# Optimization experiments

Hardware: AMD Instinct MI355X
Metric: run time of the kernel (lower is better)

The kernel has to match this reference:

```python
import jax, jax.numpy as jnp
import numpy as np

N = 8000          # nodes
E = 256000        # edges (avg_degree 32)
C = 64            # channels (num_channel == num_channel_hidden)
R = 8             # num_radial_basis
H = 64            # radial MLP hidden width
NPATH = 11        # (l1,l2)->lout Cartesian tensor-product paths
AVG_NUM_NEIGHBORS = 32.0


def setup_inputs() -> dict:
    key = jax.random.key(0)
    ks = jax.random.split(key, 19)
    rn = lambda k, shp, s=1.0: jax.random.normal(k, shp, dtype=jnp.float32) * s
    inp = {
        # node features per irrep order r: [N, C, (3,)*r]
        't0': rn(ks[0], (N, C)),
        't1': rn(ks[1], (N, C, 3)),
        't2': rn(ks[2], (N, C, 3, 3)),
        # edge Cartesian attrs per order l1
        'a0': rn(ks[3], (E,)),
        'a1': rn(ks[4], (E, 3)),
        'a2': rn(ks[5], (E, 3, 3)),
        'edge_feats': rn(ks[6], (E, R)),
        'cutoff': jax.random.uniform(ks[7], (E, 1), dtype=jnp.float32),
        # linear_up (SelfInteraction) channel-mix weights per l
        'W0': rn(ks[8], (C, C), 1.0 / np.sqrt(C)),
        'W1': rn(ks[9], (C, C), 1.0 / np.sqrt(C)),
        'W2': rn(ks[10], (C, C), 1.0 / np.sqrt(C)),
        # radial MLP: R -> H -> H -> H -> NPATH*C
        'Wr0': rn(ks[11], (R, H), 1.0 / np.sqrt(R)),
        'Wr1': rn(ks[12], (H, H), 1.0 / np.sqrt(H)),
        'Wr2': rn(ks[13], (H, H), 1.0 / np.sqrt(H)),
        'Wr3': rn(ks[14], (H, NPATH * C), 1.0 / np.sqrt(H)),
        # ICTD symmetrization matrices D_{l,l,1}: [3^l, 3^l] buffers
        'D0': rn(ks[15], (1, 1)),
        'D1': rn(ks[16], (3, 3)),
        'D2': rn(ks[17], (9, 9)),
        'edge_index': jax.random.randint(ks[18], (2, E), 0, N),
    }
    return inp


def reference(t0, t1, t2, a0, a1, a2, edge_feats, cutoff,
              W0, W1, W2, Wr0, Wr1, Wr2, Wr3, D0, D1, D2, edge_index):
    src, dst = edge_index[0], edge_index[1]

    # linear_up: per-irrep channel mixing
    u0 = jnp.einsum('nc,cd->nd', t0, W0)
    u1 = jnp.einsum('nci,cd->ndi', t1, W1)
    u2 = jnp.einsum('ncij,cd->ndij', t2, W2)

    # gather sender features per edge
    s0, s1, s2 = u0[src], u1[src], u2[src]

    # radial_net: per-edge path weights, gated by cutoff
    h = jax.nn.silu(edge_feats @ Wr0)
    h = jax.nn.silu(h @ Wr1)
    h = jax.nn.silu(h @ Wr2)
    w = ((h @ Wr3) * cutoff).reshape(E, NPATH, C)
    w = jnp.moveaxis(w, 1, 0)  # [NPATH, E, C]

    # Cartesian tensor-product paths (l1=edge attr order, l2=node feat order)
    # lout = 0 paths
    e0 = (w[0] * (a0[:, None] * s0)
          + w[1] * jnp.einsum('ei,eci->ec', a1, s1)
          + w[2] * jnp.einsum('eij,ecij->ec', a2, s2))
    # lout = 1 paths
    e1 = (w[3][..., None] * (a1[:, None, :] * s0[..., None])
          + w[4][..., None] * (a0[:, None, None] * s1)
          + w[5][..., None] * jnp.einsum('eij,ecj->eci', a2, s1)
          + w[6][..., None] * jnp.einsum('ej,ecij->eci', a1, s2))
    # lout = 2 paths
    e2 = (w[7][..., None, None] * jnp.einsum('ei,ecj->ecij', a1, s1)
          + w[8][..., None, None] * (a2[:, None] * s0[..., None, None])
          + w[9][..., None, None] * (a0[:, None, None, None] * s2)
          + w[10][..., None, None] * jnp.einsum('eik,eckj->ecij', a2, s2))

    # scatter-add to target nodes, normalize by avg_num_neighbors
    m0 = jax.ops.segment_sum(e0, dst, num_segments=N) / AVG_NUM_NEIGHBORS
    m1 = jax.ops.segment_sum(e1, dst, num_segments=N) / AVG_NUM_NEIGHBORS
    m2 = jax.ops.segment_sum(e2, dst, num_segments=N) / AVG_NUM_NEIGHBORS

    # apply D_{l,l,1} symmetrization on flattened last dims
    m0 = (m0.reshape(N, C, 1) @ D0).reshape(N, C)
    m1 = jnp.einsum('nci,ij->ncj', m1, D1)
    m2 = (m2.reshape(N, C, 9) @ D2).reshape(N, C, 3, 3)
    return (m0, m1, m2)
```

## Files before the change

kernel.cpp:

```cpp
#include <hip/hip_runtime.h>


#define NN 8000
#define NE 256000
#define OFF1 512000
#define OFF2 2048000

typedef __attribute__((ext_vector_type(8))) short short8;
typedef __attribute__((ext_vector_type(4))) float f32x4;
typedef __attribute__((ext_vector_type(2))) unsigned int uint2v;

__device__ __forceinline__ float silu_f(float x) {
    return x / (1.f + __expf(-x));
}
__device__ __forceinline__ unsigned short f2bf(float x) {
    unsigned int u = __float_as_uint(x);
    u += 0x7fff + ((u >> 16) & 1);
    return (unsigned short)(u >> 16);
}
__device__ __forceinline__ float bf2f(short x) {
    return __uint_as_float(((unsigned int)(unsigned short)x) << 16);
}

__global__ void k_prep(const int* __restrict__ ei, int* __restrict__ counts,
                       const float* __restrict__ Wr3, unsigned short* __restrict__ wr3t,
                       const float* __restrict__ Wr1, const float* __restrict__ Wr2,
                       unsigned short* __restrict__ wr1t, unsigned short* __restrict__ wr2t) {
    int b = blockIdx.x;
    if (b < 1000) {
        int e = b * 256 + threadIdx.x;
        atomicAdd(&counts[ei[NE + e]], 1);
    } else if (b < 1176) {
        int idx = (b - 1000) * 256 + threadIdx.x;
        if (idx < 704 * 64) {
            int n = idx >> 6, h = idx & 63;
            wr3t[idx] = f2bf(Wr3[h * 704 + n]);
        }
    } else {
        int idx = (b - 1176) * 256 + threadIdx.x;
        if (idx < 4096) {
            int j = idx >> 6, q = idx & 63;
            wr1t[idx] = f2bf(Wr1[q * 64 + j]);
            wr2t[idx] = f2bf(Wr2[q * 64 + j]);
        }
    }
}

__global__ __launch_bounds__(1024) void k_scan(const int* __restrict__ counts,
                                               int* __restrict__ row_ptr,
                                               int* __restrict__ cursor) {
    __shared__ int ssum[1024];
    int tid = threadIdx.x;
    int base = tid * 8;
    int v[8];
    int s = 0;
#pragma unroll
    for (int i = 0; i < 8; ++i) {
        int g = base + i;
        int x = (g < NN) ? counts[g] : 0;
        v[i] = s;
        s += x;
    }
    ssum[tid] = s;
    __syncthreads();
    for (int off = 1; off < 1024; off <<= 1) {
        int t = (tid >= off) ? ssum[tid - off] : 0;
        __syncthreads();
        ssum[tid] += t;
        __syncthreads();
    }
    int excl = ssum[tid] - s;
#pragma unroll
    for (int i = 0; i < 8; ++i) {
        int g = base + i;
        if (g < NN) {
            int val = excl + v[i];
            row_ptr[g] = val;
            cursor[g]  = val;
        }
    }
    if (tid == 0) row_ptr[NN] = NE;
}

__global__ void k_scatter(const int* __restrict__ ei, int* __restrict__ cursor,
                          int* __restrict__ sorted_eid) {
    int e = blockIdx.x * 256 + threadIdx.x;
    if (e < NE) {
        int pos = atomicAdd(&cursor[ei[NE + e]], 1);
        sorted_eid[pos] = e;
    }
}

__global__ __launch_bounds__(256) void k_linear_up(
    const float* __restrict__ t0, const float* __restrict__ t1,
    const float* __restrict__ t2, const float* __restrict__ W0,
    const float* __restrict__ W1, const float* __restrict__ W2,
    unsigned short* __restrict__ u16) {
    int lane = threadIdx.x & 63;
    int n = blockIdx.x * 4 + (threadIdx.x >> 6);
    if (n >= NN) return;
    float acc[13];
#pragma unroll
    for (int i = 0; i < 13; ++i) acc[i] = 0.f;
    const float* t0r = t0 + n * 64;
    const float* t1r = t1 + n * 192;
    const float* t2r = t2 + n * 576;
    for (int cin = 0; cin < 64; ++cin) {
        float w0 = W0[cin * 64 + lane];
        float w1 = W1[cin * 64 + lane];
        float w2 = W2[cin * 64 + lane];
        acc[0] = fmaf(t0r[cin], w0, acc[0]);
#pragma unroll
        for (int i = 0; i < 3; ++i)
            acc[1 + i] = fmaf(t1r[cin * 3 + i], w1, acc[1 + i]);
#pragma unroll
        for (int q = 0; q < 9; ++q)
            acc[4 + q] = fmaf(t2r[cin * 9 + q], w2, acc[4 + q]);
    }
    short8 lo, hi;
#pragma unroll
    for (int m = 0; m < 8; ++m) lo[m] = (short)f2bf(acc[m]);
#pragma unroll
    for (int m = 8; m < 13; ++m) hi[m - 8] = (short)f2bf(acc[m]);
    hi[5] = 0; hi[6] = 0; hi[7] = 0;
    short8* dst = (short8*)(u16 + (size_t)n * 1024 + lane * 16);
    dst[0] = lo;
    dst[1] = hi;
}

__global__ __launch_bounds__(256) void k_mlp(
    const int* __restrict__ sorted, const int* __restrict__ ei,
    const float* __restrict__ ef, const float* __restrict__ cut,
    const float* __restrict__ a0, const float* __restrict__ a1,
    const float* __restrict__ a2, const float* __restrict__ Wr0,
    const unsigned short* __restrict__ wr1t, const unsigned short* __restrict__ wr2t,
    unsigned short* __restrict__ h3s, float* __restrict__ a_s,
    int* __restrict__ src_s) {
    __shared__ __attribute__((aligned(16))) unsigned short h1[64 * 64];
    __shared__ __attribute__((aligned(16))) unsigned short h2[64 * 64];
    __shared__ int eid_l[64];
    __shared__ float cut_l[64];
    int tid = threadIdx.x;
    int c = tid & 63, sg = tid >> 6, jb = sg * 16;
    int l15 = c & 15, lg = c >> 4;
    int i0 = blockIdx.x * 64;

    if (tid < 64) {
        int eid = sorted[i0 + tid];
        eid_l[tid] = eid;
        src_s[i0 + tid] = ei[eid];
        cut_l[tid] = cut[eid];
    }
    __syncthreads();
    for (int idx = tid; idx < 64 * 13; idx += 256) {
        int k = idx / 13, m = idx - 13 * k;
        int eid = eid_l[k];
        float v = (m == 0) ? a0[eid]
                : (m < 4)  ? a1[(size_t)eid * 3 + (m - 1)]
                           : a2[(size_t)eid * 9 + (m - 4)];
        a_s[(size_t)(i0 + k) * 16 + m] = v;
    }
    for (int idx = tid; idx < 64 * 3; idx += 256) {
        int k = idx / 3, m = 13 + (idx - 3 * k);
        a_s[(size_t)(i0 + k) * 16 + m] = 0.f;
    }

    short8 W1f[4][2], W2f[4][2];
#pragma unroll
    for (int mt = 0; mt < 4; ++mt)
#pragma unroll
        for (int kf = 0; kf < 2; ++kf) {
            W1f[mt][kf] = *(const short8*)(wr1t + (mt * 16 + l15) * 64 + kf * 32 + lg * 8);
            W2f[mt][kf] = *(const short8*)(wr2t + (mt * 16 + l15) * 64 + kf * 32 + lg * 8);
        }

    {
        int eid = eid_l[c];
        const float* er = ef + (size_t)eid * 8;
        float ev[8];
#pragma unroll
        for (int r = 0; r < 8; ++r) ev[r] = er[r];
        float acc[16];
#pragma unroll
        for (int j = 0; j < 16; ++j) acc[j] = 0.f;
#pragma unroll
        for (int r = 0; r < 8; ++r)
#pragma unroll
            for (int j = 0; j < 16; ++j)
                acc[j] = fmaf(ev[r], Wr0[r * 64 + jb + j], acc[j]);
        int sw = (c & 7) << 4;
#pragma unroll
        for (int g = 0; g < 4; ++g) {
            uint2v pk;
            pk[0] = (unsigned int)f2bf(silu_f(acc[4 * g]))
                  | ((unsigned int)f2bf(silu_f(acc[4 * g + 1])) << 16);
            pk[1] = (unsigned int)f2bf(silu_f(acc[4 * g + 2]))
                  | ((unsigned int)f2bf(silu_f(acc[4 * g + 3])) << 16);
            int byte = (c * 128 + (jb + 4 * g) * 2) ^ sw;
            *(uint2v*)((char*)h1 + byte) = pk;
        }
    }
    __syncthreads();

    int e = sg * 16 + l15;
    int rb = e * 128;
    int sw = (e & 7) << 4;
    float cv = cut_l[e];
    {
        short8 B0 = *(const short8*)((char*)h1 + ((rb + lg * 16) ^ sw));
        short8 B1 = *(const short8*)((char*)h1 + ((rb + 64 + lg * 16) ^ sw));
        f32x4 d0 = {0.f, 0.f, 0.f, 0.f}, d1 = {0.f, 0.f, 0.f, 0.f};
        f32x4 d2 = {0.f, 0.f, 0.f, 0.f}, d3 = {0.f, 0.f, 0.f, 0.f};
        d0 = __builtin_amdgcn_mfma_f32_16x16x32_bf16(W1f[0][0], B0, d0, 0, 0, 0);
        d0 = __builtin_amdgcn_mfma_f32_16x16x32_bf16(W1f[0][1], B1, d0, 0, 0, 0);
        d1 = __builtin_amdgcn_mfma_f32_16x16x32_bf16(W1f[1][0], B0, d1, 0, 0, 0);
        d1 = __builtin_amdgcn_mfma_f32_16x16x32_bf16(W1f[1][1], B1, d1, 0, 0, 0);
        d2 = __builtin_amdgcn_mfma_f32_16x16x32_bf16(W1f[2][0], B0, d2, 0, 0, 0);
        d2 = __builtin_amdgcn_mfma_f32_16x16x32_bf16(W1f[2][1], B1, d2, 0, 0, 0);
        d3 = __builtin_amdgcn_mfma_f32_16x16x32_bf16(W1f[3][0], B0, d3, 0, 0, 0);
        d3 = __builtin_amdgcn_mfma_f32_16x16x32_bf16(W1f[3][1], B1, d3, 0, 0, 0);
        f32x4 dd[4] = {d0, d1, d2, d3};
#pragma unroll
        for (int mt = 0; mt < 4; ++mt) {
            uint2v pk;
            pk[0] = (unsigned int)f2bf(silu_f(dd[mt][0]))
                  | ((unsigned int)f2bf(silu_f(dd[mt][1])) << 16);
            pk[1] = (unsigned int)f2bf(silu_f(dd[mt][2]))
                  | ((unsigned int)f2bf(silu_f(dd[mt][3])) << 16);
            int byte = (rb + (mt * 16 + lg * 4) * 2) ^ sw;
            *(uint2v*)((char*)h2 + byte) = pk;
        }
    }
    {
        short8 B0 = *(const short8*)((char*)h2 + ((rb + lg * 16) ^ sw));
        short8 B1 = *(const short8*)((char*)h2 + ((rb + 64 + lg * 16) ^ sw));
        f32x4 d0 = {0.f, 0.f, 0.f, 0.f}, d1 = {0.f, 0.f, 0.f, 0.f};
        f32x4 d2 = {0.f, 0.f, 0.f, 0.f}, d3 = {0.f, 0.f, 0.f, 0.f};
        d0 = __builtin_amdgcn_mfma_f32_16x16x32_bf16(W2f[0][0], B0, d0, 0, 0, 0);
        d0 = __builtin_amdgcn_mfma_f32_16x16x32_bf16(W2f[0][1], B1, d0, 0, 0, 0);
        d1 = __builtin_amdgcn_mfma_f32_16x16x32_bf16(W2f[1][0], B0, d1, 0, 0, 0);
        d1 = __builtin_amdgcn_mfma_f32_16x16x32_bf16(W2f[1][1], B1, d1, 0, 0, 0);
        d2 = __builtin_amdgcn_mfma_f32_16x16x32_bf16(W2f[2][0], B0, d2, 0, 0, 0);
        d2 = __builtin_amdgcn_mfma_f32_16x16x32_bf16(W2f[2][1], B1, d2, 0, 0, 0);
        d3 = __builtin_amdgcn_mfma_f32_16x16x32_bf16(W2f[3][0], B0, d3, 0, 0, 0);
        d3 = __builtin_amdgcn_mfma_f32_16x16x32_bf16(W2f[3][1], B1, d3, 0, 0, 0);
        f32x4 dd[4] = {d0, d1, d2, d3};
#pragma unroll
        for (int mt = 0; mt < 4; ++mt) {
            uint2v pk;
            pk[0] = (unsigned int)f2bf(silu_f(dd[mt][0]) * cv)
                  | ((unsigned int)f2bf(silu_f(dd[mt][1]) * cv) << 16);
            pk[1] = (unsigned int)f2bf(silu_f(dd[mt][2]) * cv)
                  | ((unsigned int)f2bf(silu_f(dd[mt][3]) * cv) << 16);
            int byte = rb + (mt * 16 + lg * 4) * 2;
            *(uint2v*)((char*)h1 + byte) = pk;
        }
    }
    __syncthreads();
    {
        short8* dst = (short8*)(h3s + (size_t)i0 * 64);
        const short8* srcp = (const short8*)h1;
#pragma unroll
        for (int i = 0; i < 2; ++i) dst[tid + 256 * i] = srcp[tid + 256 * i];
    }
}

__global__ __launch_bounds__(256) void k_main(
    const unsigned short* __restrict__ u16, const int* __restrict__ row_ptr,
    const unsigned short* __restrict__ h3s, const float* __restrict__ a_s,
    const int* __restrict__ src_s, const unsigned short* __restrict__ wr3t,
    const float* __restrict__ D0, const float* __restrict__ D1,
    const float* __restrict__ D2, float* __restrict__ out) {
    __shared__ float red[4 * 13 * 64];
    __shared__ float m_l[13 * 64];

    int tid = threadIdx.x;
    int c = tid & 63;
    int sg = tid >> 6;
    int l15 = c & 15;
    int lg = c >> 4;
    int n = blockIdx.x;
    int beg = row_ptr[n], end = row_ptr[n + 1];
    int last = end - 1;

    int p0, p1, p2;
    if (sg == 0)      { p0 = 0; p1 = 3;  p2 = 8;  }
    else if (sg == 1) { p0 = 1; p1 = 4;  p2 = 7;  }
    else if (sg == 2) { p0 = 2; p1 = 9;  p2 = 6;  }
    else              { p0 = 5; p1 = 10; p2 = 10; }

    for (int cg = 0; cg < 4; ++cg) {
        int c_lane = cg * 16 + l15;
        const unsigned short* b0 = wr3t + (size_t)(p0 * 64 + c_lane) * 64 + lg * 8;
        const unsigned short* b1 = wr3t + (size_t)(p1 * 64 + c_lane) * 64 + lg * 8;
        const unsigned short* b2 = wr3t + (size_t)(p2 * 64 + c_lane) * 64 + lg * 8;

        float accm[13];
#pragma unroll
        for (int i = 0; i < 13; ++i) accm[i] = 0.f;

        for (int tb = beg; tb < end; tb += 16) {
            int rowc = min(tb + l15, last);
            const short8* ap = (const short8*)(h3s + (size_t)rowc * 64);
            short8 Af0 = ap[lg];
            short8 Af1 = ap[4 + lg];
            short8 Bf00 = *(const short8*)(b0);
            short8 Bf01 = *(const short8*)(b0 + 32);
            short8 Bf10 = *(const short8*)(b1);
            short8 Bf11 = *(const short8*)(b1 + 32);
            short8 Bf20 = *(const short8*)(b2);
            short8 Bf21 = *(const short8*)(b2 + 32);
            int gbase = tb + lg * 4;
            int gpc[4];
            short8 ulo[4];
#pragma unroll
            for (int r = 0; r < 4; ++r) {
                gpc[r] = min(gbase + r, last);
                ulo[r] = *(const short8*)(
                    u16 + (size_t)src_s[gpc[r]] * 1024 + c_lane * 16);
            }
            f32x4 w0v = {0.f, 0.f, 0.f, 0.f};
            f32x4 w1v = {0.f, 0.f, 0.f, 0.f};
            f32x4 w2v = {0.f, 0.f, 0.f, 0.f};
            w0v = __builtin_amdgcn_mfma_f32_16x16x32_bf16(Af0, Bf00, w0v, 0, 0, 0);
            w0v = __builtin_amdgcn_mfma_f32_16x16x32_bf16(Af1, Bf01, w0v, 0, 0, 0);
            w1v = __builtin_amdgcn_mfma_f32_16x16x32_bf16(Af0, Bf10, w1v, 0, 0, 0);
            w1v = __builtin_amdgcn_mfma_f32_16x16x32_bf16(Af1, Bf11, w1v, 0, 0, 0);
            w2v = __builtin_amdgcn_mfma_f32_16x16x32_bf16(Af0, Bf20, w2v, 0, 0, 0);
            w2v = __builtin_amdgcn_mfma_f32_16x16x32_bf16(Af1, Bf21, w2v, 0, 0, 0);
#pragma unroll
            for (int r = 0; r < 4; ++r) {
                int gp = gbase + r;
                float cv = (gp < end) ? 1.f : 0.f;
                float w0 = w0v[r] * cv;
                float w1 = w1v[r] * cv;
                float w2 = w2v[r] * cv;
                const unsigned short* uptr =
                    u16 + (size_t)src_s[gpc[r]] * 1024 + c_lane * 16;
                short8 ul = ulo[r];
                const float* av = a_s + (size_t)gpc[r] * 16;
                f32x4 q0 = *(const f32x4*)(av);
                f32x4 q1 = *(const f32x4*)(av + 4);
                f32x4 q2 = *(const f32x4*)(av + 8);
                float q3 = av[12];
                float ar[13] = {q0[0], q0[1], q0[2], q0[3],
                                q1[0], q1[1], q1[2], q1[3],
                                q2[0], q2[1], q2[2], q2[3], q3};
                if (sg == 0) {
                    float s0v = bf2f(ul[0]);
                    accm[0] = fmaf(w0 * ar[0], s0v, accm[0]);
#pragma unroll
                    for (int i3 = 0; i3 < 3; ++i3)
                        accm[1 + i3] = fmaf(w1 * ar[1 + i3], s0v, accm[1 + i3]);
#pragma unroll
                    for (int q = 0; q < 9; ++q)
                        accm[4 + q] = fmaf(w2 * ar[4 + q], s0v, accm[4 + q]);
                } else if (sg == 1) {
                    float s1v[3] = { bf2f(ul[1]), bf2f(ul[2]), bf2f(ul[3]) };
                    float d = ar[1] * s1v[0] + ar[2] * s1v[1] + ar[3] * s1v[2];
                    accm[0] = fmaf(w0, d, accm[0]);
                    float a0v = ar[0];
#pragma unroll
                    for (int i3 = 0; i3 < 3; ++i3)
                        accm[1 + i3] = fmaf(w1 * a0v, s1v[i3], accm[1 + i3]);
#pragma unroll
                    for (int i3 = 0; i3 < 3; ++i3)
#pragma unroll
                        for (int j3 = 0; j3 < 3; ++j3)
                            accm[4 + 3 * i3 + j3] =
                                fmaf(w2 * ar[1 + i3], s1v[j3], accm[4 + 3 * i3 + j3]);
                } else if (sg == 2) {
                    short8 uh = *(const short8*)(uptr + 8);
                    float s2v[9];
#pragma unroll
                    for (int q = 0; q < 9; ++q)
                        s2v[q] = (q < 4) ? bf2f(ul[4 + q]) : bf2f(uh[q - 4]);
                    float d = 0.f;
#pragma unroll
                    for (int q = 0; q < 9; ++q) d = fmaf(ar[4 + q], s2v[q], d);
                    accm[0] = fmaf(w0, d, accm[0]);
                    float a0v = ar[0];
#pragma unroll
                    for (int q = 0; q < 9; ++q)
                        accm[4 + q] = fmaf(w1 * a0v, s2v[q], accm[4 + q]);
#pragma unroll
                    for (int i3 = 0; i3 < 3; ++i3) {
                        float t = ar[1] * s2v[3 * i3] + ar[2] * s2v[3 * i3 + 1] +
                                  ar[3] * s2v[3 * i3 + 2];
                        accm[1 + i3] = fmaf(w2, t, accm[1 + i3]);
                    }
                } else {
                    short8 uh = *(const short8*)(uptr + 8);
                    float s1v[3] = { bf2f(ul[1]), bf2f(ul[2]), bf2f(ul[3]) };
                    float s2v[9];
#pragma unroll
                    for (int q = 0; q < 9; ++q)
                        s2v[q] = (q < 4) ? bf2f(ul[4 + q]) : bf2f(uh[q - 4]);
#pragma unroll
                    for (int i3 = 0; i3 < 3; ++i3) {
                        float t = ar[4 + 3 * i3] * s1v[0] + ar[4 + 3 * i3 + 1] * s1v[1] +
                                  ar[4 + 3 * i3 + 2] * s1v[2];
                        accm[1 + i3] = fmaf(w0, t, accm[1 + i3]);
                    }
#pragma unroll
                    for (int i3 = 0; i3 < 3; ++i3)
#pragma unroll
                        for (int j3 = 0; j3 < 3; ++j3) {
                            float t = ar[4 + 3 * i3] * s2v[j3] +
                                      ar[4 + 3 * i3 + 1] * s2v[3 + j3] +
                                      ar[4 + 3 * i3 + 2] * s2v[6 + j3];
                            accm[4 + 3 * i3 + j3] = fmaf(w1, t, accm[4 + 3 * i3 + j3]);
                        }
                }
            }
        }
#pragma unroll
        for (int m = 0; m < 13; ++m) {
            float v = accm[m];
            v += __shfl_xor(v, 16, 64);
            v += __shfl_xor(v, 32, 64);
            if (lg == 0) red[(sg * 13 + m) * 64 + c_lane] = v;
        }
    }

    __syncthreads();
    for (int m = sg; m < 13; m += 4) {
        float s = red[m * 64 + c] + red[(13 + m) * 64 + c] +
                  red[(26 + m) * 64 + c] + red[(39 + m) * 64 + c];
        m_l[m * 64 + c] = s * (1.f / 32.f);
    }
    __syncthreads();
    if (sg == 0) {
        out[n * 64 + c] = m_l[c] * D0[0];
    } else if (sg == 1) {
        float v0 = m_l[64 + c], v1 = m_l[128 + c], v2 = m_l[192 + c];
#pragma unroll
        for (int j = 0; j < 3; ++j) {
            float s = v0 * D1[j] + v1 * D1[3 + j] + v2 * D1[6 + j];
            out[OFF1 + (n * 64 + c) * 3 + j] = s;
        }
    } else {
        float v[9];
#pragma unroll
        for (int p = 0; p < 9; ++p) v[p] = m_l[(4 + p) * 64 + c];
        int q0 = (sg == 2) ? 0 : 5;
        int q1 = (sg == 2) ? 5 : 9;
        for (int q = q0; q < q1; ++q) {
            float s = 0.f;
#pragma unroll
            for (int p = 0; p < 9; ++p) s = fmaf(v[p], D2[p * 9 + q], s);
            out[OFF2 + (n * 64 + c) * 9 + q] = s;
        }
    }
}

extern "C" void kernel_launch(void* const* d_in, const int* in_sizes, int n_in,
                              void* d_out, int out_size, void* d_ws, size_t ws_size,
                              hipStream_t stream) {
    const float* t0 = (const float*)d_in[0];
    const float* t1 = (const float*)d_in[1];
    const float* t2 = (const float*)d_in[2];
    const float* a0 = (const float*)d_in[3];
    const float* a1 = (const float*)d_in[4];
    const float* a2 = (const float*)d_in[5];
    const float* ef = (const float*)d_in[6];
    const float* cut = (const float*)d_in[7];
    const float* W0 = (const float*)d_in[8];
    const float* W1 = (const float*)d_in[9];
    const float* W2 = (const float*)d_in[10];
    const float* Wr0 = (const float*)d_in[11];
    const float* Wr1 = (const float*)d_in[12];
    const float* Wr2 = (const float*)d_in[13];
    const float* Wr3 = (const float*)d_in[14];
    const float* D0 = (const float*)d_in[15];
    const float* D1 = (const float*)d_in[16];
    const float* D2 = (const float*)d_in[17];
    const int* ei = (const int*)d_in[18];
    float* out = (float*)d_out;

    unsigned short* u16 = (unsigned short*)d_ws;
    unsigned short* h3s = u16 + (size_t)NN * 1024;
    float* a_s = (float*)(h3s + (size_t)NE * 64);
    int* src_s = (int*)(a_s + (size_t)NE * 16);
    int* counts = src_s + NE;
    int* row_ptr = counts + NN;
    int* cursor = row_ptr + NN + 1;
    int* sorted = cursor + NN;
    unsigned short* wr3t = (unsigned short*)(sorted + NE);
    unsigned short* wr1t = wr3t + 45056;
    unsigned short* wr2t = wr1t + 4096;

    hipMemsetAsync(counts, 0, NN * sizeof(int), stream);
    k_prep<<<1192, 256, 0, stream>>>(ei, counts, Wr3, wr3t, Wr1, Wr2, wr1t, wr2t);
    k_scan<<<1, 1024, 0, stream>>>(counts, row_ptr, cursor);
    k_scatter<<<(NE + 255) / 256, 256, 0, stream>>>(ei, cursor, sorted);
    k_linear_up<<<NN / 4, 256, 0, stream>>>(t0, t1, t2, W0, W1, W2, u16);
    k_mlp<<<NE / 64, 256, 0, stream>>>(sorted, ei, ef, cut, a0, a1, a2,
                                       Wr0, wr1t, wr2t, h3s, a_s, src_s);
    k_main<<<NN, 256, 0, stream>>>(u16, row_ptr, h3s, a_s, src_s, wr3t,
                                   D0, D1, D2, out);
}
```

Baseline: 622.0 us.

## Split channels across waves instead of paths to remove cross-wave reduction

Each wave now owns a 16-channel group and computes all 11 paths for it, where before each wave handled a subset of paths and looped over all four channel groups. This removes the 4x channel-group loop, the redundant per-wave gathers of edge attributes and sender features, and the shared-memory cross-wave reduction with its extra barrier. In exchange each wave issues 22 MFMAs per edge tile and holds more weight fragments live, which raises register pressure. Wave-divergent branching on the wave index is gone.

Measured after the change: 595.8 us. -4.2%, faster.

```diff
diff --git a/kernel.cpp b/kernel.cpp
--- a/kernel.cpp
+++ b/kernel.cpp
@@ -271,7 +271,6 @@
     const int* __restrict__ src_s, const unsigned short* __restrict__ wr3t,
     const float* __restrict__ D0, const float* __restrict__ D1,
     const float* __restrict__ D2, float* __restrict__ out) {
-    __shared__ float red[4 * 13 * 64];
     __shared__ float m_l[13 * 64];
 
     int tid = threadIdx.x;
@@ -282,154 +281,149 @@
     int n = blockIdx.x;
     int beg = row_ptr[n], end = row_ptr[n + 1];
     int last = end - 1;
-
-    int p0, p1, p2;
-    if (sg == 0)      { p0 = 0; p1 = 3;  p2 = 8;  }
-    else if (sg == 1) { p0 = 1; p1 = 4;  p2 = 7;  }
-    else if (sg == 2) { p0 = 2; p1 = 9;  p2 = 6;  }
-    else              { p0 = 5; p1 = 10; p2 = 10; }
-
-    for (int cg = 0; cg < 4; ++cg) {
-        int c_lane = cg * 16 + l15;
-        const unsigned short* b0 = wr3t + (size_t)(p0 * 64 + c_lane) * 64 + lg * 8;
-        const unsigned short* b1 = wr3t + (size_t)(p1 * 64 + c_lane) * 64 + lg * 8;
-        const unsigned short* b2 = wr3t + (size_t)(p2 * 64 + c_lane) * 64 + lg * 8;
-
-        float accm[13];
-#pragma unroll
-        for (int i = 0; i < 13; ++i) accm[i] = 0.f;
-
-        for (int tb = beg; tb < end; tb += 16) {
-            int rowc = min(tb + l15, last);
-            const short8* ap = (const short8*)(h3s + (size_t)rowc * 64);
-            short8 Af0 = ap[lg];
-            short8 Af1 = ap[4 + lg];
-            short8 Bf00 = *(const short8*)(b0);
-            short8 Bf01 = *(const short8*)(b0 + 32);
-            short8 Bf10 = *(const short8*)(b1);
-            short8 Bf11 = *(const short8*)(b1 + 32);
-            short8 Bf20 = *(const short8*)(b2);
-            short8 Bf21 = *(const short8*)(b2 + 32);
-            int gbase = tb + lg * 4;
-            int gpc[4];
-            short8 ulo[4];
-#pragma unroll
-            for (int r = 0; r < 4; ++r) {
-                gpc[r] = min(gbase + r, last);
-                ulo[r] = *(const short8*)(
-                    u16 + (size_t)src_s[gpc[r]] * 1024 + c_lane * 16);
+    int c_lane = sg * 16 + l15;
+
+    float accm[13];
+#pragma unroll
+    for (int i = 0; i < 13; ++i) accm[i] = 0.f;
+
+    for (int tb = beg; tb < end; tb += 16) {
+        int rowc = min(tb + l15, last);
+        const short8* ap = (const short8*)(h3s + (size_t)rowc * 64);
+        short8 Af0 = ap[lg];
+        short8 Af1 = ap[4 + lg];
+        int gbase = tb + lg * 4;
+        int gpc[4];
+        short8 ulo[4];
+#pragma unroll
+        for (int r = 0; r < 4; ++r) {
+            gpc[r] = min(gbase + r, last);
+            ulo[r] = *(const short8*)(
+                u16 + (size_t)src_s[gpc[r]] * 1024 + c_lane * 16);
+        }
+
+        const int PA[6] = {0, 1, 3, 4, 5, 7};
+        f32x4 wA[6];
+#pragma unroll
+        for (int ip = 0; ip < 6; ++ip) {
+            const unsigned short* bp =
+                wr3t + (size_t)(PA[ip] * 64 + c_lane) * 64 + lg * 8;
+            short8 B0 = *(const short8*)(bp);
+            short8 B1 = *(const short8*)(bp + 32);
+            f32x4 acc = {0.f, 0.f, 0.f, 0.f};
+            acc = __builtin_amdgcn_mfma_f32_16x16x32_bf16(Af0, B0, acc, 0, 0, 0);
+            acc = __builtin_amdgcn_mfma_f32_16x16x32_bf16(Af1, B1, acc, 0, 0, 0);
+            wA[ip] = acc;
+        }
+#pragma unroll
+        for (int r = 0; r < 4; ++r) {
+            int gp = gbase + r;
+            float cv = (gp < end) ? 1.f : 0.f;
+            const float* av = a_s + (size_t)gpc[r] * 16;
+            f32x4 q0 = *(const f32x4*)(av);
+            f32x4 q1 = *(const f32x4*)(av + 4);
+            f32x4 q2 = *(const f32x4*)(av + 8);
+            float q3 = av[12];
+            float ar[13] = {q0[0], q0[1], q0[2], q0[3],
+                            q1[0], q1[1], q1[2], q1[3],
+                            q2[0], q2[1], q2[2], q2[3], q3};
+            short8 ul = ulo[r];
+            float s0 = bf2f(ul[0]);
+            float s1v[3] = { bf2f(ul[1]), bf2f(ul[2]), bf2f(ul[3]) };
+            float w0 = wA[0][r] * cv, w1 = wA[1][r] * cv, w3 = wA[2][r] * cv;
+            float w4 = wA[3][r] * cv, w5 = wA[4][r] * cv, w7 = wA[5][r] * cv;
+            accm[0] = fmaf(w0 * ar[0], s0, accm[0]);
+            float d1 = ar[1] * s1v[0] + ar[2] * s1v[1] + ar[3] * s1v[2];
+            accm[0] = fmaf(w1, d1, accm[0]);
+#pragma unroll
+            for (int i3 = 0; i3 < 3; ++i3) {
+                accm[1 + i3] = fmaf(w3 * ar[1 + i3], s0, accm[1 + i3]);
+                accm[1 + i3] = fmaf(w4 * ar[0], s1v[i3], accm[1 + i3]);
+                float t5 = ar[4 + 3 * i3] * s1v[0] + ar[4 + 3 * i3 + 1] * s1v[1] +
+                           ar[4 + 3 * i3 + 2] * s1v[2];
+                accm[1 + i3] = fmaf(w5, t5, accm[1 + i3]);
+#pragma unroll
+                for (int j3 = 0; j3 < 3; ++j3)
+                    accm[4 + 3 * i3 + j3] =
+                        fmaf(w7 * ar[1 + i3], s1v[j3], accm[4 + 3 * i3 + j3]);
             }
-            f32x4 w0v = {0.f, 0.f, 0.f, 0.f};
-            f32x4 w1v = {0.f, 0.f, 0.f, 0.f};
-            f32x4 w2v = {0.f, 0.f, 0.f, 0.f};
-            w0v = __builtin_amdgcn_mfma_f32_16x16x32_bf16(Af0, Bf00, w0v, 0, 0, 0);
-            w0v = __builtin_amdgcn_mfma_f32_16x16x32_bf16(Af1, Bf01, w0v, 0, 0, 0);
-            w1v = __builtin_amdgcn_mfma_f32_16x16x32_bf16(Af0, Bf10, w1v, 0, 0, 0);
-            w1v = __builtin_amdgcn_mfma_f32_16x16x32_bf16(Af1, Bf11, w1v, 0, 0, 0);
-            w2v = __builtin_amdgcn_mfma_f32_16x16x32_bf16(Af0, Bf20, w2v, 0, 0, 0);
-            w2v = __builtin_amdgcn_mfma_f32_16x16x32_bf16(Af1, Bf21, w2v, 0, 0, 0);
-#pragma unroll
-            for (int r = 0; r < 4; ++r) {
-                int gp = gbase + r;
-                float cv = (gp < end) ? 1.f : 0.f;
-                float w0 = w0v[r] * cv;
-                float w1 = w1v[r] * cv;
-                float w2 = w2v[r] * cv;
-                const unsigned short* uptr =
-                    u16 + (size_t)src_s[gpc[r]] * 1024 + c_lane * 16;
-                short8 ul = ulo[r];
-                const float* av = a_s + (size_t)gpc[r] * 16;
-                f32x4 q0 = *(const f32x4*)(av);
-                f32x4 q1 = *(const f32x4*)(av + 4);
-                f32x4 q2 = *(const f32x4*)(av + 8);
-                float q3 = av[12];
-                float ar[13] = {q0[0], q0[1], q0[2], q0[3],
-                                q1[0], q1[1], q1[2], q1[3],
-                                q2[0], q2[1], q2[2], q2[3], q3};
-                if (sg == 0) {
-                    float s0v = bf2f(ul[0]);
-                    accm[0] = fmaf(w0 * ar[0], s0v, accm[0]);
-#pragma unroll
-                    for (int i3 = 0; i3 < 3; ++i3)
-                        accm[1 + i3] = fmaf(w1 * ar[1 + i3], s0v, accm[1 + i3]);
-#pragma unroll
-                    for (int q = 0; q < 9; ++q)
-                        accm[4 + q] = fmaf(w2 * ar[4 + q], s0v, accm[4 + q]);
-                } else if (sg == 1) {
-                    float s1v[3] = { bf2f(ul[1]), bf2f(ul[2]), bf2f(ul[3]) };
-                    float d = ar[1] * s1v[0] + ar[2] * s1v[1] + ar[3] * s1v[2];
-                    accm[0] = fmaf(w0, d, accm[0]);
-                    float a0v = ar[0];
-#pragma unroll
-                    for (int i3 = 0; i3 < 3; ++i3)
-                        accm[1 + i3] = fmaf(w1 * a0v, s1v[i3], accm[1 + i3]);
-#pragma unroll
-                    for (int i3 = 0; i3 < 3; ++i3)
-#pragma unroll
-                        for (int j3 = 0; j3 < 3; ++j3)
-                            accm[4 + 3 * i3 + j3] =
-                                fmaf(w2 * ar[1 + i3], s1v[j3], accm[4 + 3 * i3 + j3]);
-                } else if (sg == 2) {
-                    short8 uh = *(const short8*)(uptr + 8);
-                    float s2v[9];
-#pragma unroll
-                    for (int q = 0; q < 9; ++q)
-                        s2v[q] = (q < 4) ? bf2f(ul[4 + q]) : bf2f(uh[q - 4]);
-                    float d = 0.f;
-#pragma unroll
-                    for (int q = 0; q < 9; ++q) d = fmaf(ar[4 + q], s2v[q], d);
-                    accm[0] = fmaf(w0, d, accm[0]);
-                    float a0v = ar[0];
-#pragma unroll
-                    for (int q = 0; q < 9; ++q)
-                        accm[4 + q] = fmaf(w1 * a0v, s2v[q], accm[4 + q]);
-#pragma unroll
-                    for (int i3 = 0; i3 < 3; ++i3) {
-                        float t = ar[1] * s2v[3 * i3] + ar[2] * s2v[3 * i3 + 1] +
-                                  ar[3] * s2v[3 * i3 + 2];
-                        accm[1 + i3] = fmaf(w2, t, accm[1 + i3]);
-                    }
-                } else {
-                    short8 uh = *(const short8*)(uptr + 8);
-                    float s1v[3] = { bf2f(ul[1]), bf2f(ul[2]), bf2f(ul[3]) };
-                    float s2v[9];
-#pragma unroll
-                    for (int q = 0; q < 9; ++q)
-                        s2v[q] = (q < 4) ? bf2f(ul[4 + q]) : bf2f(uh[q - 4]);
-#pragma unroll
-                    for (int i3 = 0; i3 < 3; ++i3) {
-                        float t = ar[4 + 3 * i3] * s1v[0] + ar[4 + 3 * i3 + 1] * s1v[1] +
-                                  ar[4 + 3 * i3 + 2] * s1v[2];
-                        accm[1 + i3] = fmaf(w0, t, accm[1 + i3]);
-                    }
-#pragma unroll
-                    for (int i3 = 0; i3 < 3; ++i3)
-#pragma unroll
-                        for (int j3 = 0; j3 < 3; ++j3) {
-                            float t = ar[4 + 3 * i3] * s2v[j3] +
-                                      ar[4 + 3 * i3 + 1] * s2v[3 + j3] +
-                                      ar[4 + 3 * i3 + 2] * s2v[6 + j3];
-                            accm[4 + 3 * i3 + j3] = fmaf(w1, t, accm[4 + 3 * i3 + j3]);
-                        }
+        }
+
+        short8 uhi[4];
+#pragma unroll
+        for (int r = 0; r < 4; ++r)
+            uhi[r] = *(const short8*)(
+                u16 + (size_t)src_s[gpc[r]] * 1024 + c_lane * 16 + 8);
+        const int PB[5] = {2, 6, 8, 9, 10};
+        f32x4 wB[5];
+#pragma unroll
+        for (int ip = 0; ip < 5; ++ip) {
+            const unsigned short* bp =
+                wr3t + (size_t)(PB[ip] * 64 + c_lane) * 64 + lg * 8;
+            short8 B0 = *(const short8*)(bp);
+            short8 B1 = *(const short8*)(bp + 32);
+            f32x4 acc = {0.f, 0.f, 0.f, 0.f};
+            acc = __builtin_amdgcn_mfma_f32_16x16x32_bf16(Af0, B0, acc, 0, 0, 0);
+            acc = __builtin_amdgcn_mfma_f32_16x16x32_bf16(Af1, B1, acc, 0, 0, 0);
+            wB[ip] = acc;
+        }
+#pragma unroll
+        for (int r = 0; r < 4; ++r) {
+            int gp = gbase + r;
+            float cv = (gp < end) ? 1.f : 0.f;
+            const float* av = a_s + (size_t)gpc[r] * 16;
+            f32x4 q0 = *(const f32x4*)(av);
+            f32x4 q1 = *(const f32x4*)(av + 4);
+            f32x4 q2 = *(const f32x4*)(av + 8);
+            float q3 = av[12];
+            float ar[13] = {q0[0], q0[1], q0[2], q0[3],
+                            q1[0], q1[1], q1[2], q1[3],
+                            q2[0], q2[1], q2[2], q2[3], q3};
+            short8 ul = ulo[r];
+            short8 uh = uhi[r];
+            float s0 = bf2f(ul[0]);
+            float s2v[9];
+#pragma unroll
+            for (int q = 0; q < 9; ++q)
+                s2v[q] = (q < 4) ? bf2f(ul[4 + q]) : bf2f(uh[q - 4]);
+            float w2 = wB[0][r] * cv, w6 = wB[1][r] * cv, w8 = wB[2][r] * cv;
+            float w9 = wB[3][r] * cv, w10 = wB[4][r] * cv;
+            float d2 = 0.f;
+#pragma unroll
+            for (int q = 0; q < 9; ++q) d2 = fmaf(ar[4 + q], s2v[q], d2);
+            accm[0] = fmaf(w2, d2, accm[0]);
+#pragma unroll
+            for (int i3 = 0; i3 < 3; ++i3) {
+                float t6 = ar[1] * s2v[3 * i3] + ar[2] * s2v[3 * i3 + 1] +
+                           ar[3] * s2v[3 * i3 + 2];
+                accm[1 + i3] = fmaf(w6, t6, accm[1 + i3]);
+            }
+#pragma unroll
+            for (int q = 0; q < 9; ++q) {
+                accm[4 + q] = fmaf(w8 * ar[4 + q], s0, accm[4 + q]);
+                accm[4 + q] = fmaf(w9 * ar[0], s2v[q], accm[4 + q]);
+            }
+#pragma unroll
+            for (int i3 = 0; i3 < 3; ++i3)
+#pragma unroll
+                for (int j3 = 0; j3 < 3; ++j3) {
+                    float t10 = ar[4 + 3 * i3] * s2v[j3] +
+                                ar[4 + 3 * i3 + 1] * s2v[3 + j3] +
+                                ar[4 + 3 * i3 + 2] * s2v[6 + j3];
+                    accm[4 + 3 * i3 + j3] = fmaf(w10, t10, accm[4 + 3 * i3 + j3]);
                 }
-            }
-        }
-#pragma unroll
-        for (int m = 0; m < 13; ++m) {
-            float v = accm[m];
-            v += __shfl_xor(v, 16, 64);
-            v += __shfl_xor(v, 32, 64);
-            if (lg == 0) red[(sg * 13 + m) * 64 + c_lane] = v;
-        }
-    }
-
+        }
+    }
+
+#pragma unroll
+    for (int m = 0; m < 13; ++m) {
+        float v = accm[m];
+        v += __shfl_xor(v, 16, 64);
+        v += __shfl_xor(v, 32, 64);
+        if (lg == 0) m_l[m * 64 + c_lane] = v * (1.f / 32.f);
+    }
     __syncthreads();
-    for (int m = sg; m < 13; m += 4) {
-        float s = red[m * 64 + c] + red[(13 + m) * 64 + c] +
-                  red[(26 + m) * 64 + c] + red[(39 + m) * 64 + c];
-        m_l[m * 64 + c] = s * (1.f / 32.f);
-    }
-    __syncthreads();
+
     if (sg == 0) {
         out[n * 64 + c] = m_l[c] * D0[0];
     } else if (sg == 1) {
```
